# Optimization experiments

Measured on AMD Instinct MI355X. Metric: run time of the kernel, lower is better.

The kernel has to match this reference:

```python
import jax, jax.numpy as jnp
import numpy as np

T = 0.07          # cfg.CAP.TEMP
K = 50            # cfg.CAP.HARD_NEG_K
LOSS_WEIGHT = 0.5 # cfg.CAP.LOSS_WEIGHT
C_CAM = 8         # number of cameras
P = 2048          # pseudo-ID classes per camera bank


def setup_inputs() -> dict:
    key = jax.random.key(0)
    k1, k2, k3, k4 = jax.random.split(key, 4)
    B, D = 256, 2048
    inputs = jax.random.normal(k1, (B, D), jnp.float32)
    labels = jax.random.randint(k2, (B,), 0, P)
    cams = jax.random.randint(k3, (B,), 0, C_CAM)
    tempV = jax.random.normal(k4, (C_CAM * P, D), jnp.float32)
    tempV = tempV / jnp.linalg.norm(tempV, axis=1, keepdims=True)  # memory rows are L2-normalized
    return {"inputs": inputs, "labels": labels, "cams": cams, "tempV": tempV}


def _seg_mean_sum(vals, cams):
    # original loops over unique cams: loss += mean(vals within cam); empty cams contribute 0
    sums = jax.ops.segment_sum(vals, cams, num_segments=C_CAM)
    cnts = jax.ops.segment_sum(jnp.ones_like(vals), cams, num_segments=C_CAM)
    return jnp.sum(jnp.where(cnts > 0, sums / jnp.maximum(cnts, 1.0), 0.0))


def reference(inputs, labels, cams, tempV):
    B = inputs.shape[0]
    # cfg.CAP.NORM_FEAT
    x = inputs / jnp.linalg.norm(inputs, axis=1, keepdims=True)

    # one fused matmul against the concatenated memory; per-camera banks are contiguous P-slices
    all_logits = x @ tempV.T                      # [B, C_CAM*P]
    logits3 = all_logits.reshape(B, C_CAM, P)

    # ---- intra-camera loss: logits against the sample's own camera bank ----
    percam = jnp.take_along_axis(logits3, cams[:, None, None], axis=1)[:, 0, :] / T  # [B, P]
    lse_i = jax.scipy.special.logsumexp(percam, axis=1)
    ce = lse_i - jnp.take_along_axis(percam, labels[:, None], axis=1)[:, 0]
    loss_intra = _seg_mean_sum(ce, cams)

    # ---- inter-camera loss with hard-negative mining ----
    rows = jnp.arange(B)[:, None]
    # each ID has one centroid in every camera bank: positions label + P*cam
    ori_ind = labels[:, None] + P * jnp.arange(C_CAM)[None, :]        # [B, C_CAM]
    sims = all_logits.at[rows, ori_ind].set(-10000.0)                 # mask positives
    _, sel_ind = jax.lax.top_k(sims, K)                               # hard negatives (== sort[-K:])
    ori_logits = jnp.take_along_axis(all_logits, ori_ind, axis=1) / T  # [B, C_CAM]
    sel_logits = jnp.take_along_axis(all_logits, sel_ind, axis=1) / T  # [B, K]
    cat = jnp.concatenate([ori_logits, sel_logits], axis=1)            # [B, C_CAM+K]
    lse_c = jax.scipy.special.logsumexp(cat, axis=1)
    # target = 1/len(ori) on positives, 0 on negatives -> lse - mean(positive logits)
    loss_k = lse_c - jnp.mean(ori_logits, axis=1)
    loss_inter = LOSS_WEIGHT * _seg_mean_sum(loss_k, cams)

    return (loss_intra, loss_inter)
```

## Files before the change

kernel.cpp:

```cpp
#include <hip/hip_runtime.h>
#include <hip/hip_bf16.h>

#define BATCH 256
#define DIM   2048
#define NMEM  16384
#define PCLS  2048
#define CCAM  8
#define KSEL  50
#define T_INV 14.285714285714285714f
#define NB2   2048

typedef __bf16 bf16x8 __attribute__((ext_vector_type(8)));
typedef float  f32x4  __attribute__((ext_vector_type(4)));

static __device__ __forceinline__ unsigned int f2bf(float f) {
  unsigned int u = __float_as_uint(f);
  return (u + 0x7FFFu + ((u >> 16) & 1u)) >> 16;
}
static __device__ __forceinline__ unsigned int pk2(float lo, float hi) {
  return f2bf(lo) | (f2bf(hi) << 16);
}
static __device__ __forceinline__ int binw(float x, float lo, float scale) {
  int b = (int)((x - lo) * scale);
  return b > (NB2 - 1) ? (NB2 - 1) : b;
}

__global__ __launch_bounds__(256) void norm_cast_kernel(
    const float* __restrict__ in, unsigned short* __restrict__ xb) {
  __shared__ float red[256];
  const int b = blockIdx.x, t = threadIdx.x;
  const float4* row = (const float4*)(in + (size_t)b * DIM);
  float4 a0 = row[t];
  float4 a1 = row[t + 256];
  float ss = a0.x*a0.x + a0.y*a0.y + a0.z*a0.z + a0.w*a0.w
           + a1.x*a1.x + a1.y*a1.y + a1.z*a1.z + a1.w*a1.w;
  red[t] = ss; __syncthreads();
  for (int s = 128; s > 0; s >>= 1) { if (t < s) red[t] += red[t + s]; __syncthreads(); }
  const float rn = rsqrtf(red[0]);
  ushort4 o0, o1;
  o0.x = (unsigned short)f2bf(a0.x*rn); o0.y = (unsigned short)f2bf(a0.y*rn);
  o0.z = (unsigned short)f2bf(a0.z*rn); o0.w = (unsigned short)f2bf(a0.w*rn);
  o1.x = (unsigned short)f2bf(a1.x*rn); o1.y = (unsigned short)f2bf(a1.y*rn);
  o1.z = (unsigned short)f2bf(a1.z*rn); o1.w = (unsigned short)f2bf(a1.w*rn);
  *(ushort4*)&xb[(size_t)b * DIM + t * 4]         = o0;
  *(ushort4*)&xb[(size_t)b * DIM + (t + 256) * 4] = o1;
}

#define BM 128
#define BN 32
#define BK 32
#define NT (DIM / BK)

__global__ __launch_bounds__(256, 2) void gemm_kernel(
    const unsigned short* __restrict__ X,
    const float* __restrict__ V,
    float* __restrict__ C) {
  __shared__ unsigned short Bs0[BN * BK];
  __shared__ unsigned short Bs1[BN * BK];
  const int t  = threadIdx.x;
  const int n0 = blockIdx.x * BN;
  const int m0 = blockIdx.y * BM;
  const int lane = t & 63;
  const int w    = t >> 6;
  const int wm   = w * 32;

  f32x4 acc[2][2];
#pragma unroll
  for (int i = 0; i < 2; i++)
#pragma unroll
    for (int j = 0; j < 2; j++) acc[i][j] = (f32x4){0.f, 0.f, 0.f, 0.f};

  const int br = t >> 3;
  const int bc = (t & 7) * 4;
  const float* Vp = V + (size_t)(n0 + br) * DIM + bc;
  unsigned short* BW0 = &Bs0[br * BK + bc];
  unsigned short* BW1 = &Bs1[br * BK + bc];

  const int fr = lane & 15;
  const int fq8 = (lane >> 4) * 8;
  const unsigned short* Ap = X + (size_t)(m0 + wm + fr) * DIM + fq8;

  {
    float4 bt = *(const float4*)Vp;
    uint2 p; p.x = pk2(bt.x, bt.y); p.y = pk2(bt.z, bt.w);
    *(uint2*)BW0 = p;
  }
  float4 bO = *(const float4*)(Vp + 1 * BK);
  float4 bE = *(const float4*)(Vp + 2 * BK);
  bf16x8 aE0 = *(const bf16x8*)(Ap);
  bf16x8 aE1 = *(const bf16x8*)(Ap + 16 * DIM);
  bf16x8 aO0 = *(const bf16x8*)(Ap + BK);
  bf16x8 aO1 = *(const bf16x8*)(Ap + 16 * DIM + BK);
  __syncthreads();

#pragma unroll 1
  for (int s = 0; s < NT / 2; ++s) {
    const int te = 2 * s;

    {
      uint2 p; p.x = pk2(bO.x, bO.y); p.y = pk2(bO.z, bO.w);
      *(uint2*)BW1 = p;
    }
    {
      const int kb = min(te + 3, NT - 1) * BK;
      bO = *(const float4*)(Vp + kb);
      const int ka = min(te + 2, NT - 1) * BK;
      bf16x8 n0f = *(const bf16x8*)(Ap + ka);
      bf16x8 n1f = *(const bf16x8*)(Ap + 16 * DIM + ka);
      bf16x8 bF0 = *(const bf16x8*)&Bs0[fr * BK + fq8];
      bf16x8 bF1 = *(const bf16x8*)&Bs0[(16 + fr) * BK + fq8];
      acc[0][0] = __builtin_amdgcn_mfma_f32_16x16x32_bf16(aE0, bF0, acc[0][0], 0, 0, 0);
      acc[0][1] = __builtin_amdgcn_mfma_f32_16x16x32_bf16(aE0, bF1, acc[0][1], 0, 0, 0);
      acc[1][0] = __builtin_amdgcn_mfma_f32_16x16x32_bf16(aE1, bF0, acc[1][0], 0, 0, 0);
      acc[1][1] = __builtin_amdgcn_mfma_f32_16x16x32_bf16(aE1, bF1, acc[1][1], 0, 0, 0);
      aE0 = n0f; aE1 = n1f;
    }
    __syncthreads();

    {
      uint2 p; p.x = pk2(bE.x, bE.y); p.y = pk2(bE.z, bE.w);
      *(uint2*)BW0 = p;
    }
    {
      const int kb = min(te + 4, NT - 1) * BK;
      bE = *(const float4*)(Vp + kb);
      const int ka = min(te + 3, NT - 1) * BK;
      bf16x8 n0f = *(const bf16x8*)(Ap + ka);
      bf16x8 n1f = *(const bf16x8*)(Ap + 16 * DIM + ka);
      bf16x8 bF0 = *(const bf16x8*)&Bs1[fr * BK + fq8];
      bf16x8 bF1 = *(const bf16x8*)&Bs1[(16 + fr) * BK + fq8];
      acc[0][0] = __builtin_amdgcn_mfma_f32_16x16x32_bf16(aO0, bF0, acc[0][0], 0, 0, 0);
      acc[0][1] = __builtin_amdgcn_mfma_f32_16x16x32_bf16(aO0, bF1, acc[0][1], 0, 0, 0);
      acc[1][0] = __builtin_amdgcn_mfma_f32_16x16x32_bf16(aO1, bF0, acc[1][0], 0, 0, 0);
      acc[1][1] = __builtin_amdgcn_mfma_f32_16x16x32_bf16(aO1, bF1, acc[1][1], 0, 0, 0);
      aO0 = n0f; aO1 = n1f;
    }
    __syncthreads();
  }

  const int cr = (lane >> 4) * 4;
  const int cc = lane & 15;
#pragma unroll
  for (int i = 0; i < 2; i++)
#pragma unroll
    for (int j = 0; j < 2; j++)
#pragma unroll
      for (int r = 0; r < 4; r++)
        C[(size_t)(m0 + wm + i * 16 + cr + r) * NMEM + (n0 + j * 16 + cc)] =
            acc[i][j][r];
}

__global__ __launch_bounds__(1024) void row_loss_kernel(
    const float* __restrict__ logits,
    const int* __restrict__ labels, const int* __restrict__ cams,
    float* __restrict__ ce_out, float* __restrict__ lossk_out) {
  __shared__ float ovs[CCAM];
  __shared__ float wredA[16], wredB[16];
  __shared__ int   hist[NB2];
  __shared__ int   pint[256];
  __shared__ float bl[512];
  __shared__ int   bcount;
  __shared__ int   bstar_s, cabove_s, totwin_s;
  __shared__ float vmax_s;

  const int b = blockIdx.x, t = threadIdx.x;
  const int lane = t & 63, wid = t >> 6;
  const int cam = cams[b], label = labels[b];
  const float* row = logits + (size_t)b * NMEM;

  if (t < CCAM) ovs[t] = row[t * PCLS + label];

  float4 rr[4];
#pragma unroll
  for (int i = 0; i < 4; i++) rr[i] = *(const float4*)(row + (size_t)(t + 1024 * i) * 4);

  float vmax = -1e30f, Si = 0.f;
#pragma unroll
  for (int i = 0; i < 4; i++) {
    const int base = (t + 1024 * i) * 4;
    const float xs[4] = {rr[i].x, rr[i].y, rr[i].z, rr[i].w};
#pragma unroll
    for (int e = 0; e < 4; e++) {
      const int n = base + e;
      const float x = xs[e];
      if ((n >> 11) == cam) Si += __expf(x * T_INV);
      if ((n & (PCLS - 1)) != label) vmax = fmaxf(vmax, x);
    }
  }
#pragma unroll
  for (int off = 32; off > 0; off >>= 1) {
    vmax = fmaxf(vmax, __shfl_down(vmax, off));
    Si  += __shfl_down(Si, off);
  }
  if (lane == 0) { wredA[wid] = vmax; wredB[wid] = Si; }
  __syncthreads();
  if (t == 0) {
    float m = -1e30f, s = 0.f;
    for (int i = 0; i < 16; i++) { m = fmaxf(m, wredA[i]); s += wredB[i]; }
    vmax_s = m;
    ce_out[b] = logf(s) - ovs[cam] * T_INV;
    bcount = 0;
  }
  __syncthreads();

  float W = 0.0625f;
  float lo = 0.f, scale = 0.f;
  for (int att = 0; att < 6; ++att) {
    __syncthreads();
    for (int i = t; i < NB2; i += 1024) hist[i] = 0;
    __syncthreads();
    lo = vmax_s - W; scale = (float)NB2 / W;
#pragma unroll
    for (int i = 0; i < 4; i++) {
      const int base = (t + 1024 * i) * 4;
      const float xs[4] = {rr[i].x, rr[i].y, rr[i].z, rr[i].w};
#pragma unroll
      for (int e = 0; e < 4; e++) {
        const int n = base + e;
        const float x = xs[e];
        if (((n & (PCLS - 1)) != label) && x >= lo)
          atomicAdd(&hist[binw(x, lo, scale)], 1);
      }
    }
    __syncthreads();
    if (t < 256) {
      int ps = 0;
#pragma unroll
      for (int i = 0; i < 8; i++) ps += hist[t * 8 + i];
      pint[t] = ps;
    }
    __syncthreads();
    if (t == 0) {
      int tot = 0;
      for (int i = 0; i < 256; i++) tot += pint[i];
      totwin_s = tot;
      if (tot >= KSEL) {
        int cum = 0, bstar = 0, cab = 0;
        for (int tc = 255; tc >= 0; tc--) {
          if (cum + pint[tc] >= KSEL) {
            for (int bi = tc * 8 + 7; bi >= tc * 8; bi--) {
              int h = hist[bi];
              if (cum + h >= KSEL) { bstar = bi; cab = cum; break; }
              cum += h;
            }
            break;
          }
          cum += pint[tc];
        }
        bstar_s = bstar; cabove_s = cab;
      }
    }
    __syncthreads();
    if (totwin_s >= KSEL) break;
    W *= 8.f;
  }
  const int bstar = bstar_s;

  float S2 = 0.f;
#pragma unroll
  for (int i = 0; i < 4; i++) {
    const int base = (t + 1024 * i) * 4;
    const float xs[4] = {rr[i].x, rr[i].y, rr[i].z, rr[i].w};
#pragma unroll
    for (int e = 0; e < 4; e++) {
      const int n = base + e;
      const float x = xs[e];
      if (((n & (PCLS - 1)) != label) && x >= lo) {
        const int bin = binw(x, lo, scale);
        if (bin > bstar) S2 += __expf(x * T_INV);
        else if (bin == bstar) {
          int p = atomicAdd(&bcount, 1);
          if (p < 512) bl[p] = x;
        }
      }
    }
  }
#pragma unroll
  for (int off = 32; off > 0; off >>= 1) S2 += __shfl_down(S2, off);
  if (lane == 0) wredB[wid] = S2;
  __syncthreads();

  if (t == 0) {
    float S2tot = 0.f;
    for (int i = 0; i < 16; i++) S2tot += wredB[i];
    const int need = KSEL - cabove_s;
    const int bc = min(bcount, 512);
    for (int r = 0; r < need; r++) {
      float mx = -1e30f; int mi = 0;
      for (int i = 0; i < bc; i++) if (bl[i] > mx) { mx = bl[i]; mi = i; }
      S2tot += __expf(mx * T_INV);
      bl[mi] = -1e30f;
    }
    float sumo = 0.f;
#pragma unroll
    for (int c = 0; c < CCAM; c++) { S2tot += __expf(ovs[c] * T_INV); sumo += ovs[c]; }
    lossk_out[b] = logf(S2tot) - (sumo * T_INV) * (1.0f / CCAM);
  }
}

__global__ __launch_bounds__(256) void finalize_kernel(
    const float* __restrict__ ce, const float* __restrict__ lossk,
    const int* __restrict__ cams, float* __restrict__ out) {
  __shared__ float ce_s[BATCH], lk_s[BATCH];
  __shared__ int   cam_s[BATCH];
  __shared__ float si[CCAM], sk[CCAM], cnt[CCAM];
  const int t = threadIdx.x;
  ce_s[t]  = ce[t];
  lk_s[t]  = lossk[t];
  cam_s[t] = cams[t];
  __syncthreads();
  if (t < CCAM) {
    float a = 0.f, b = 0.f; int n = 0;
    for (int i = 0; i < BATCH; i++) {
      if (cam_s[i] == t) { a += ce_s[i]; b += lk_s[i]; n++; }
    }
    si[t] = a; sk[t] = b; cnt[t] = (float)n;
  }
  __syncthreads();
  if (t == 0) {
    float li = 0.f, lk = 0.f;
    for (int c = 0; c < CCAM; c++) {
      if (cnt[c] > 0.f) { li += si[c] / cnt[c]; lk += sk[c] / cnt[c]; }
    }
    out[0] = li;
    out[1] = 0.5f * lk;
  }
}

extern "C" void kernel_launch(void* const* d_in, const int* in_sizes, int n_in,
                              void* d_out, int out_size, void* d_ws, size_t ws_size,
                              hipStream_t stream) {
  const float* inputs = (const float*)d_in[0];
  const int*   labels = (const int*)d_in[1];
  const int*   cams   = (const int*)d_in[2];
  const float* tempV  = (const float*)d_in[3];
  float* out = (float*)d_out;

  char* ws = (char*)d_ws;
  unsigned short* xb  = (unsigned short*)ws;
  float* logits       = (float*)(ws + (1u << 20));
  float* ce           = (float*)(ws + (1u << 20) + (16u << 20));
  float* lossk        = (float*)(ws + (1u << 20) + (16u << 20) + 1024);

  norm_cast_kernel<<<BATCH, 256, 0, stream>>>(inputs, xb);
  gemm_kernel<<<dim3(NMEM / BN, BATCH / BM), 256, 0, stream>>>(xb, tempV, logits);
  row_loss_kernel<<<BATCH, 1024, 0, stream>>>(logits, labels, cams, ce, lossk);
  finalize_kernel<<<1, 256, 0, stream>>>(ce, lossk, cams, out);
}
```

Baseline: 286.5 us.

## Pre-pack X into MFMA fragment layout and restructure GEMM to full-M blocks

The normalize/cast kernel now writes X in a fragment-packed layout, so each lane's bf16x8 A operand is one contiguous, coalesced load. The GEMM is restructured so each block covers all 256 rows against 16 memory rows, with each warp doing 64 rows. V is staged in large 512-wide K chunks with a padded LDS stride, and the A fragments are streamed straight from global memory. This removes the duplicate V reads across M-blocks and cuts the barrier count. In exchange it relies on A being served from cache with heavier per-lane global loads, and launch bounds are raised to 3 blocks per SM.

```diff
diff --git a/kernel.cpp b/kernel.cpp
--- a/kernel.cpp
+++ b/kernel.cpp
@@ -25,8 +25,15 @@
   return b > (NB2 - 1) ? (NB2 - 1) : b;
 }
 
+static __device__ __forceinline__ size_t pa_idx(int r, int c) {
+  return (size_t)(r >> 4) * (size_t)(64 * 8 * (DIM / 32))
+       + (size_t)(c >> 5) * 512
+       + (size_t)(((r & 15) | (((c >> 3) & 3) << 4))) * 8
+       + (size_t)(c & 7);
+}
+
 __global__ __launch_bounds__(256) void norm_cast_kernel(
-    const float* __restrict__ in, unsigned short* __restrict__ xb) {
+    const float* __restrict__ in, unsigned short* __restrict__ xpk) {
   __shared__ float red[256];
   const int b = blockIdx.x, t = threadIdx.x;
   const float4* row = (const float4*)(in + (size_t)b * DIM);
@@ -42,98 +49,92 @@
   o0.z = (unsigned short)f2bf(a0.z*rn); o0.w = (unsigned short)f2bf(a0.w*rn);
   o1.x = (unsigned short)f2bf(a1.x*rn); o1.y = (unsigned short)f2bf(a1.y*rn);
   o1.z = (unsigned short)f2bf(a1.z*rn); o1.w = (unsigned short)f2bf(a1.w*rn);
-  *(ushort4*)&xb[(size_t)b * DIM + t * 4]         = o0;
-  *(ushort4*)&xb[(size_t)b * DIM + (t + 256) * 4] = o1;
-}
-
-#define BM 128
-#define BN 32
-#define BK 32
-#define NT (DIM / BK)
-
-__global__ __launch_bounds__(256, 2) void gemm_kernel(
-    const unsigned short* __restrict__ X,
+  *(ushort4*)&xpk[pa_idx(b, 4 * t)]         = o0;
+  *(ushort4*)&xpk[pa_idx(b, 4 * (t + 256))] = o1;
+}
+
+#define BN  16
+#define QK  512
+#define LDB 516
+
+__global__ __launch_bounds__(256, 3) void gemm_kernel(
+    const unsigned short* __restrict__ Xpk,
     const float* __restrict__ V,
     float* __restrict__ C) {
-  __shared__ unsigned short Bs0[BN * BK];
-  __shared__ unsigned short Bs1[BN * BK];
-  const int t  = threadIdx.x;
-  const int n0 = blockIdx.x * BN;
-  const int m0 = blockIdx.y * BM;
+  __shared__ unsigned short Bs0[BN * LDB];
+  __shared__ unsigned short Bs1[BN * LDB];
+  const int t = threadIdx.x;
   const int lane = t & 63;
   const int w    = t >> 6;
-  const int wm   = w * 32;
-
-  f32x4 acc[2][2];
-#pragma unroll
-  for (int i = 0; i < 2; i++)
-#pragma unroll
-    for (int j = 0; j < 2; j++) acc[i][j] = (f32x4){0.f, 0.f, 0.f, 0.f};
-
-  const int br = t >> 3;
-  const int bc = (t & 7) * 4;
-  const float* Vp = V + (size_t)(n0 + br) * DIM + bc;
-  unsigned short* BW0 = &Bs0[br * BK + bc];
-  unsigned short* BW1 = &Bs1[br * BK + bc];
-
-  const int fr = lane & 15;
+  const int n0 = blockIdx.x * BN;
+
+  const int sr = t >> 4;
+  const int sc = (t & 15) * 4;
+  const float* Vp = V + (size_t)(n0 + sr) * DIM + sc;
+  unsigned short* Bw0 = &Bs0[sr * LDB + sc];
+  unsigned short* Bw1 = &Bs1[sr * LDB + sc];
+
+  const int fr  = lane & 15;
   const int fq8 = (lane >> 4) * 8;
-  const unsigned short* Ap = X + (size_t)(m0 + wm + fr) * DIM + fq8;
+  const unsigned short* Ap = Xpk + (size_t)(w * 4) * 32768 + (size_t)lane * 8;
+
+  f32x4 acc[4];
+#pragma unroll
+  for (int i = 0; i < 4; i++) acc[i] = (f32x4){0.f, 0.f, 0.f, 0.f};
 
   {
-    float4 bt = *(const float4*)Vp;
-    uint2 p; p.x = pk2(bt.x, bt.y); p.y = pk2(bt.z, bt.w);
-    *(uint2*)BW0 = p;
-  }
-  float4 bO = *(const float4*)(Vp + 1 * BK);
-  float4 bE = *(const float4*)(Vp + 2 * BK);
-  bf16x8 aE0 = *(const bf16x8*)(Ap);
-  bf16x8 aE1 = *(const bf16x8*)(Ap + 16 * DIM);
-  bf16x8 aO0 = *(const bf16x8*)(Ap + BK);
-  bf16x8 aO1 = *(const bf16x8*)(Ap + 16 * DIM + BK);
-  __syncthreads();
-
-#pragma unroll 1
-  for (int s = 0; s < NT / 2; ++s) {
-    const int te = 2 * s;
-
-    {
-      uint2 p; p.x = pk2(bO.x, bO.y); p.y = pk2(bO.z, bO.w);
-      *(uint2*)BW1 = p;
-    }
-    {
-      const int kb = min(te + 3, NT - 1) * BK;
-      bO = *(const float4*)(Vp + kb);
-      const int ka = min(te + 2, NT - 1) * BK;
-      bf16x8 n0f = *(const bf16x8*)(Ap + ka);
-      bf16x8 n1f = *(const bf16x8*)(Ap + 16 * DIM + ka);
-      bf16x8 bF0 = *(const bf16x8*)&Bs0[fr * BK + fq8];
-      bf16x8 bF1 = *(const bf16x8*)&Bs0[(16 + fr) * BK + fq8];
-      acc[0][0] = __builtin_amdgcn_mfma_f32_16x16x32_bf16(aE0, bF0, acc[0][0], 0, 0, 0);
-      acc[0][1] = __builtin_amdgcn_mfma_f32_16x16x32_bf16(aE0, bF1, acc[0][1], 0, 0, 0);
-      acc[1][0] = __builtin_amdgcn_mfma_f32_16x16x32_bf16(aE1, bF0, acc[1][0], 0, 0, 0);
-      acc[1][1] = __builtin_amdgcn_mfma_f32_16x16x32_bf16(aE1, bF1, acc[1][1], 0, 0, 0);
-      aE0 = n0f; aE1 = n1f;
-    }
-    __syncthreads();
-
-    {
-      uint2 p; p.x = pk2(bE.x, bE.y); p.y = pk2(bE.z, bE.w);
-      *(uint2*)BW0 = p;
-    }
-    {
-      const int kb = min(te + 4, NT - 1) * BK;
-      bE = *(const float4*)(Vp + kb);
-      const int ka = min(te + 3, NT - 1) * BK;
-      bf16x8 n0f = *(const bf16x8*)(Ap + ka);
-      bf16x8 n1f = *(const bf16x8*)(Ap + 16 * DIM + ka);
-      bf16x8 bF0 = *(const bf16x8*)&Bs1[fr * BK + fq8];
-      bf16x8 bF1 = *(const bf16x8*)&Bs1[(16 + fr) * BK + fq8];
-      acc[0][0] = __builtin_amdgcn_mfma_f32_16x16x32_bf16(aO0, bF0, acc[0][0], 0, 0, 0);
-      acc[0][1] = __builtin_amdgcn_mfma_f32_16x16x32_bf16(aO0, bF1, acc[0][1], 0, 0, 0);
-      acc[1][0] = __builtin_amdgcn_mfma_f32_16x16x32_bf16(aO1, bF0, acc[1][0], 0, 0, 0);
-      acc[1][1] = __builtin_amdgcn_mfma_f32_16x16x32_bf16(aO1, bF1, acc[1][1], 0, 0, 0);
-      aO0 = n0f; aO1 = n1f;
+    float4 vs[8];
+#pragma unroll
+    for (int g = 0; g < 8; g++) vs[g] = *(const float4*)(Vp + g * 64);
+#pragma unroll
+    for (int g = 0; g < 8; g++) {
+      uint2 p; p.x = pk2(vs[g].x, vs[g].y); p.y = pk2(vs[g].z, vs[g].w);
+      *(uint2*)(Bw0 + g * 64) = p;
+    }
+  }
+  __syncthreads();
+
+#pragma unroll
+  for (int q = 0; q < 4; ++q) {
+    const unsigned short* rb = (q & 1) ? Bs1 : Bs0;
+    unsigned short*       wb = (q & 1) ? Bw0 : Bw1;
+    const int kcb = q * 16;
+
+    bf16x8 aE[4], aO[4], bE, bO;
+    float4 vs[8];
+    bE = *(const bf16x8*)&rb[fr * LDB + fq8];
+#pragma unroll
+    for (int i = 0; i < 4; ++i)
+      aE[i] = *(const bf16x8*)(Ap + (size_t)i * 32768 + (size_t)kcb * 512);
+
+#pragma unroll
+    for (int j = 0; j < 16; j += 2) {
+      if (q < 3)
+        vs[j >> 1] = *(const float4*)(Vp + (q + 1) * QK + (j >> 1) * 64);
+      bO = *(const bf16x8*)&rb[fr * LDB + (j + 1) * 32 + fq8];
+#pragma unroll
+      for (int i = 0; i < 4; ++i)
+        aO[i] = *(const bf16x8*)(Ap + (size_t)i * 32768 + (size_t)(kcb + j + 1) * 512);
+#pragma unroll
+      for (int i = 0; i < 4; ++i)
+        acc[i] = __builtin_amdgcn_mfma_f32_16x16x32_bf16(aE[i], bE, acc[i], 0, 0, 0);
+      if (j < 14) {
+        bE = *(const bf16x8*)&rb[fr * LDB + (j + 2) * 32 + fq8];
+#pragma unroll
+        for (int i = 0; i < 4; ++i)
+          aE[i] = *(const bf16x8*)(Ap + (size_t)i * 32768 + (size_t)(kcb + j + 2) * 512);
+      }
+#pragma unroll
+      for (int i = 0; i < 4; ++i)
+        acc[i] = __builtin_amdgcn_mfma_f32_16x16x32_bf16(aO[i], bO, acc[i], 0, 0, 0);
+    }
+
+    if (q < 3) {
+#pragma unroll
+      for (int g = 0; g < 8; ++g) {
+        uint2 p; p.x = pk2(vs[g].x, vs[g].y); p.y = pk2(vs[g].z, vs[g].w);
+        *(uint2*)(wb + g * 64) = p;
+      }
     }
     __syncthreads();
   }
@@ -141,13 +142,10 @@
   const int cr = (lane >> 4) * 4;
   const int cc = lane & 15;
 #pragma unroll
-  for (int i = 0; i < 2; i++)
-#pragma unroll
-    for (int j = 0; j < 2; j++)
-#pragma unroll
-      for (int r = 0; r < 4; r++)
-        C[(size_t)(m0 + wm + i * 16 + cr + r) * NMEM + (n0 + j * 16 + cc)] =
-            acc[i][j][r];
+  for (int i = 0; i < 4; i++)
+#pragma unroll
+    for (int r = 0; r < 4; r++)
+      C[(size_t)(w * 64 + i * 16 + cr + r) * NMEM + (n0 + cc)] = acc[i][r];
 }
 
 __global__ __launch_bounds__(1024) void row_loss_kernel(
@@ -337,13 +335,13 @@
   float* out = (float*)d_out;
 
   char* ws = (char*)d_ws;
-  unsigned short* xb  = (unsigned short*)ws;
+  unsigned short* xpk = (unsigned short*)ws;
   float* logits       = (float*)(ws + (1u << 20));
   float* ce           = (float*)(ws + (1u << 20) + (16u << 20));
   float* lossk        = (float*)(ws + (1u << 20) + (16u << 20) + 1024);
 
-  norm_cast_kernel<<<BATCH, 256, 0, stream>>>(inputs, xb);
-  gemm_kernel<<<dim3(NMEM / BN, BATCH / BM), 256, 0, stream>>>(xb, tempV, logits);
+  norm_cast_kernel<<<BATCH, 256, 0, stream>>>(inputs, xpk);
+  gemm_kernel<<<NMEM / BN, 256, 0, stream>>>(xpk, tempV, logits);
   row_loss_kernel<<<BATCH, 1024, 0, stream>>>(logits, labels, cams, ce, lossk);
   finalize_kernel<<<1, 256, 0, stream>>>(ce, lossk, cams, out);
 }
```

After: 270.3 us. -5.7%, faster.
